# Performance work log

Measured on AMD Instinct MI355X. Metric: run time of the kernel, lower is better.

Reference implementation:

```python
import jax, jax.numpy as jnp
import numpy as np
import math

B, L, C, H, W = 2, 8, 64, 64, 33
M1, M2 = 16, 16


def setup_inputs() -> dict:
    key = jax.random.key(0)
    ks = jax.random.split(key, 6)
    scale = 1.0 / math.sqrt(C)
    shp_x = (B, L, C, H, W)
    shp_w = (C, C, M1, M2)
    return {
        "x_real": jax.random.normal(ks[0], shp_x, jnp.float32),
        "x_imag": jax.random.normal(ks[1], shp_x, jnp.float32),
        "wr1": scale * jax.random.normal(ks[2], shp_w, jnp.float32),
        "wi1": scale * jax.random.normal(ks[3], shp_w, jnp.float32),
        "wr2": scale * jax.random.normal(ks[4], shp_w, jnp.float32),
        "wi2": scale * jax.random.normal(ks[5], shp_w, jnp.float32),
    }


def _cmul_einsum(xr, xi, wr, wi):
    # complex einsum 'blcxy,ocxy->bloxy' expressed in real arithmetic
    or_ = jnp.einsum('blcxy,ocxy->bloxy', xr, wr) - jnp.einsum('blcxy,ocxy->bloxy', xi, wi)
    oi_ = jnp.einsum('blcxy,ocxy->bloxy', xr, wi) + jnp.einsum('blcxy,ocxy->bloxy', xi, wr)
    return or_, oi_


def reference(x_real, x_imag, wr1, wi1, wr2, wi2):
    m1 = min(H, M1)
    m2 = min(W, M2)
    # corner 1: low positive frequencies
    o1r, o1i = _cmul_einsum(x_real[:, :, :, :m1, :m2], x_imag[:, :, :, :m1, :m2],
                            wr1[:, :, :m1, :m2], wi1[:, :, :m1, :m2])
    out_r = jnp.zeros((B, L, C, H, W), jnp.float32).at[:, :, :, :m1, :m2].set(o1r)
    out_i = jnp.zeros((B, L, C, H, W), jnp.float32).at[:, :, :, :m1, :m2].set(o1i)
    if H > 1:
        # corner 2: high (negative) frequencies along H
        o2r, o2i = _cmul_einsum(x_real[:, :, :, -m1:, :m2], x_imag[:, :, :, -m1:, :m2],
                                wr2[:, :, :m1, :m2], wi2[:, :, :m1, :m2])
        out_r = out_r.at[:, :, :, -m1:, :m2].set(o2r)
        out_i = out_i.at[:, :, :, -m1:, :m2].set(o2i)
    # stack real/imag (equivalent to the complex output of the torch module)
    return jnp.stack([out_r, out_i], axis=0)
```

## Files before the change

kernel.cpp:

```cpp
#include <hip/hip_runtime.h>


constexpr int Cc    = 64;
constexpr int Hh    = 64;
constexpr int Ww    = 33;
constexpr int BL    = 16;
constexpr int HW    = Hh * Ww;
constexpr int PLANE = Cc * HW;
constexpr int TOT   = BL * PLANE;
constexpr int WSTR  = Cc * 16 * 16;

__global__ __launch_bounds__(256) void spectral_fused_kernel(
    const float* __restrict__ xr, const float* __restrict__ xi,
    const float* __restrict__ wr1, const float* __restrict__ wi1,
    const float* __restrict__ wr2, const float* __restrict__ wi2,
    float* __restrict__ out)
{
    const int bid = blockIdx.x;
    const int t   = threadIdx.x;

    if (bid < 2048) {
        const int oq     = bid & 3;
        const int blidx  = (bid >> 2) & 15;
        const int xrow   = (bid >> 6) & 15;
        const int corner = bid >> 10;

        const int y = t & 15;
        const int o = oq * 16 + (t >> 4);

        const float* wr = corner ? wr2 : wr1;
        const float* wi = corner ? wi2 : wi1;
        const int xin = corner ? (48 + xrow) : xrow;

        const float* xrp = xr + blidx * PLANE + xin * Ww + y;
        const float* xip = xi + blidx * PLANE + xin * Ww + y;
        const float* wrp = wr + o * WSTR + xrow * 16 + y;
        const float* wip = wi + o * WSTR + xrow * 16 + y;

        float or_ = 0.f, oi_ = 0.f;
        #pragma unroll 8
        for (int c = 0; c < Cc; ++c) {
            const float a   = xrp[c * HW];
            const float b   = xip[c * HW];
            const float wre = wrp[c * 256];
            const float wim = wip[c * 256];
            or_ = fmaf(a,  wre, or_);
            or_ = fmaf(-b, wim, or_);
            oi_ = fmaf(a,  wim, oi_);
            oi_ = fmaf(b,  wre, oi_);
        }

        const size_t oidx = (size_t)(blidx * Cc + o) * HW + (size_t)xin * Ww + y;
        out[oidx]       = or_;
        out[TOT + oidx] = oi_;

        const size_t rowbase0 = (size_t)(blidx * Cc + oq * 16) * HW + (size_t)xin * Ww;
        #pragma unroll
        for (int k = t; k < 544; k += 256) {
            const int ri  = k >= 272;
            const int rem = ri ? (k - 272) : k;
            const int ol  = rem / 17;
            const int yy  = 16 + rem % 17;
            const size_t idx = rowbase0 + (size_t)ol * HW + yy + (ri ? (size_t)TOT : 0);
            out[idx] = 0.f;
        }
    } else {
        const int p = bid - 2048;
        const int ri = p >> 10;
        const int plane = p & 1023;
        float4* dst = (float4*)(out + (size_t)ri * TOT + (size_t)plane * HW + 528);
        const float4 z = make_float4(0.f, 0.f, 0.f, 0.f);
        dst[t] = z;
        if (t < 8) dst[256 + t] = z;
    }
}

extern "C" void kernel_launch(void* const* d_in, const int* in_sizes, int n_in,
                              void* d_out, int out_size, void* d_ws, size_t ws_size,
                              hipStream_t stream) {
    const float* xr  = (const float*)d_in[0];
    const float* xi  = (const float*)d_in[1];
    const float* wr1 = (const float*)d_in[2];
    const float* wi1 = (const float*)d_in[3];
    const float* wr2 = (const float*)d_in[4];
    const float* wi2 = (const float*)d_in[5];
    float* out = (float*)d_out;

    spectral_fused_kernel<<<4096, 256, 0, stream>>>(xr, xi, wr1, wi1, wr2, wi2, out);
}
```

Baseline: 111.3 us.

## Stage x slice in shared memory and compute 4 outputs per thread

Compute blocks now cover four batch-layer slices each and first stage the needed x rows (real and imaginary, all 64 channels) into a 32KB shared buffer. Each thread then computes four adjacent y outputs using float4 weight loads and float4 shared reads. Weights are reused across four batch slices per block. This cuts compute blocks from 2048 to 512. The cost is a shared-memory staging step with a barrier, lower occupancy from the 32KB of LDS per block, and scalar scattered output stores.

```diff
diff --git a/kernel.cpp b/kernel.cpp
--- a/kernel.cpp
+++ b/kernel.cpp
@@ -2,12 +2,10 @@
 
 
 constexpr int Cc    = 64;
-constexpr int Hh    = 64;
 constexpr int Ww    = 33;
-constexpr int BL    = 16;
-constexpr int HW    = Hh * Ww;
+constexpr int HW    = 64 * Ww;
 constexpr int PLANE = Cc * HW;
-constexpr int TOT   = BL * PLANE;
+constexpr int TOT   = 16 * PLANE;
 constexpr int WSTR  = Cc * 16 * 16;
 
 __global__ __launch_bounds__(256) void spectral_fused_kernel(
@@ -19,54 +17,86 @@
     const int bid = blockIdx.x;
     const int t   = threadIdx.x;
 
-    if (bid < 2048) {
+    if (bid < 512) {
         const int oq     = bid & 3;
-        const int blidx  = (bid >> 2) & 15;
-        const int xrow   = (bid >> 6) & 15;
-        const int corner = bid >> 10;
+        const int blq    = (bid >> 2) & 3;
+        const int xrow   = (bid >> 4) & 15;
+        const int corner = bid >> 8;
+        const int xin    = corner ? (48 + xrow) : xrow;
+        const float* wr  = corner ? wr2 : wr1;
+        const float* wi  = corner ? wi2 : wi1;
 
-        const int y = t & 15;
-        const int o = oq * 16 + (t >> 4);
+        __shared__ __align__(16) float xs[8192];
 
-        const float* wr = corner ? wr2 : wr1;
-        const float* wi = corner ? wi2 : wi1;
-        const int xin = corner ? (48 + xrow) : xrow;
+        {
+            const int y  = t & 15;
+            const int wb = (t >> 4) & 3;
+            const int cg = t >> 6;
+            const int src_base = (blq * 4 + wb) * PLANE + xin * Ww + y;
+            #pragma unroll
+            for (int k = 0; k < 32; ++k) {
+                const int r = k >> 4;
+                const int c = ((k & 15) << 2) | cg;
+                const float* src = (r ? xi : xr) + (size_t)src_base + c * HW;
+                xs[r * 4096 + c * 64 + wb * 16 + y] = *src;
+            }
+        }
+        __syncthreads();
 
-        const float* xrp = xr + blidx * PLANE + xin * Ww + y;
-        const float* xip = xi + blidx * PLANE + xin * Ww + y;
-        const float* wrp = wr + o * WSTR + xrow * 16 + y;
-        const float* wip = wi + o * WSTR + xrow * 16 + y;
+        const int yq  = t & 3;
+        const int blj = (t >> 2) & 3;
+        const int ol  = t >> 4;
+        const int o   = oq * 16 + ol;
+        const int bl  = blq * 4 + blj;
 
-        float or_ = 0.f, oi_ = 0.f;
+        const float* wrp = wr + o * WSTR + xrow * 16 + yq * 4;
+        const float* wip = wi + o * WSTR + xrow * 16 + yq * 4;
+        const float4* xsr = reinterpret_cast<const float4*>(xs) + blj * 4 + yq;
+        const float4* xsi = xsr + 1024;
+
+        float4 ar = make_float4(0.f, 0.f, 0.f, 0.f);
+        float4 ai = make_float4(0.f, 0.f, 0.f, 0.f);
+
         #pragma unroll 8
         for (int c = 0; c < Cc; ++c) {
-            const float a   = xrp[c * HW];
-            const float b   = xip[c * HW];
-            const float wre = wrp[c * 256];
-            const float wim = wip[c * 256];
-            or_ = fmaf(a,  wre, or_);
-            or_ = fmaf(-b, wim, or_);
-            oi_ = fmaf(a,  wim, oi_);
-            oi_ = fmaf(b,  wre, oi_);
+            const float4 wre = *reinterpret_cast<const float4*>(wrp + c * 256);
+            const float4 wim = *reinterpret_cast<const float4*>(wip + c * 256);
+            const float4 a   = xsr[c * 16];
+            const float4 b   = xsi[c * 16];
+            ar.x = fmaf(a.x, wre.x, ar.x); ar.x = fmaf(-b.x, wim.x, ar.x);
+            ai.x = fmaf(a.x, wim.x, ai.x); ai.x = fmaf( b.x, wre.x, ai.x);
+            ar.y = fmaf(a.y, wre.y, ar.y); ar.y = fmaf(-b.y, wim.y, ar.y);
+            ai.y = fmaf(a.y, wim.y, ai.y); ai.y = fmaf( b.y, wre.y, ai.y);
+            ar.z = fmaf(a.z, wre.z, ar.z); ar.z = fmaf(-b.z, wim.z, ar.z);
+            ai.z = fmaf(a.z, wim.z, ai.z); ai.z = fmaf( b.z, wre.z, ai.z);
+            ar.w = fmaf(a.w, wre.w, ar.w); ar.w = fmaf(-b.w, wim.w, ar.w);
+            ai.w = fmaf(a.w, wim.w, ai.w); ai.w = fmaf( b.w, wre.w, ai.w);
         }
 
-        const size_t oidx = (size_t)(blidx * Cc + o) * HW + (size_t)xin * Ww + y;
-        out[oidx]       = or_;
-        out[TOT + oidx] = oi_;
+        const size_t ob = (size_t)(bl * Cc + o) * HW + xin * Ww + yq * 4;
+        out[ob + 0] = ar.x; out[ob + 1] = ar.y;
+        out[ob + 2] = ar.z; out[ob + 3] = ar.w;
+        out[TOT + ob + 0] = ai.x; out[TOT + ob + 1] = ai.y;
+        out[TOT + ob + 2] = ai.z; out[TOT + ob + 3] = ai.w;
 
-        const size_t rowbase0 = (size_t)(blidx * Cc + oq * 16) * HW + (size_t)xin * Ww;
         #pragma unroll
-        for (int k = t; k < 544; k += 256) {
-            const int ri  = k >= 272;
-            const int rem = ri ? (k - 272) : k;
-            const int ol  = rem / 17;
-            const int yy  = 16 + rem % 17;
-            const size_t idx = rowbase0 + (size_t)ol * HW + yy + (ri ? (size_t)TOT : 0);
-            out[idx] = 0.f;
+        for (int q = 0; q < 9; ++q) {
+            const int k = t + q * 256;
+            if (k < 2176) {
+                const int ri   = k >= 1088;
+                const int rem  = ri ? (k - 1088) : k;
+                const int ol_  = rem / 68;
+                const int sub  = rem - ol_ * 68;
+                const int blj_ = sub / 17;
+                const int yy   = 16 + (sub - blj_ * 17);
+                const size_t idx = (size_t)((blq * 4 + blj_) * Cc + oq * 16 + ol_) * HW
+                                 + (size_t)xin * Ww + yy + (ri ? (size_t)TOT : 0);
+                out[idx] = 0.f;
+            }
         }
     } else {
-        const int p = bid - 2048;
-        const int ri = p >> 10;
+        const int p     = bid - 512;
+        const int ri    = p >> 10;
         const int plane = p & 1023;
         float4* dst = (float4*)(out + (size_t)ri * TOT + (size_t)plane * HW + 528);
         const float4 z = make_float4(0.f, 0.f, 0.f, 0.f);
@@ -86,5 +116,5 @@
     const float* wi2 = (const float*)d_in[5];
     float* out = (float*)d_out;
 
-    spectral_fused_kernel<<<4096, 256, 0, stream>>>(xr, xi, wr1, wi1, wr2, wi2, out);
+    spectral_fused_kernel<<<2560, 256, 0, stream>>>(xr, xi, wr1, wi1, wr2, wi2, out);
 }
```

New measurement: 93.43 us. 1.19x faster.
